# Optimization experiments

Hardware: AMD Instinct MI355X
Metric: run time of the kernel (lower is better)

## Reference

```python
import jax, jax.numpy as jnp
import numpy as np
from functools import partial

# Gate order along axis 0 of Wi/bi/Wh/bh: 0=r (input gate), 1=f (forget), 2=g (cell), 3=o (output)

def setup_inputs() -> dict:
    key = jax.random.key(0)
    ks = jax.random.split(key, 6)
    B, T, V, E, H, O = 64, 512, 32000, 256, 512, 1
    s_e, s_h = 1.0 / np.sqrt(E), 1.0 / np.sqrt(H)
    return {
        "input_words": jax.random.randint(ks[0], (B, T), 0, V, dtype=jnp.int64),
        "emb": jax.random.normal(ks[1], (V, E), dtype=jnp.float32) * 0.02,
        "Wi": jax.random.normal(ks[2], (4, H, E), dtype=jnp.float32) * s_e,
        "bi": jnp.zeros((4, H), dtype=jnp.float32),
        "Wh": jax.random.normal(ks[3], (4, H, H), dtype=jnp.float32) * s_h,
        "bh": jnp.zeros((4, H), dtype=jnp.float32),
        "Wfc": jax.random.normal(ks[4], (O, H), dtype=jnp.float32) * s_h,
        "bfc": jnp.zeros((O,), dtype=jnp.float32),
    }


def reference(input_words, emb, Wi, bi, Wh, bh, Wfc, bfc):
    B, T = input_words.shape
    H = Wh.shape[-1]
    x = emb[input_words]                     # [B, T, E]
    # Precompute input projections for all 4 gates, all timesteps: one big GEMM.
    xg = jnp.einsum('bte,ghe->tbgh', x, Wi) + bi  # [T, B, 4, H]

    def step(carry, xg_t):
        h, c = carry
        gates = xg_t + jnp.einsum('bk,ghk->bgh', h, Wh) + bh  # [B, 4, H]
        r = jax.nn.sigmoid(gates[:, 0])
        f = jax.nn.sigmoid(gates[:, 1])
        g = jnp.tanh(gates[:, 2])
        o = jax.nn.sigmoid(gates[:, 3])
        c = f * c + r * g
        h = o * jnp.tanh(c)
        return (h, c), None

    h0 = jnp.zeros((B, H), dtype=x.dtype)
    c0 = jnp.zeros((B, H), dtype=x.dtype)
    (h, c), _ = jax.lax.scan(step, (h0, c0), xg)
    out = jax.nn.sigmoid(h @ Wfc.T + bfc)    # [B, n_output]
    return (out, h)
```

## Files before the change

kernel.cpp:

```cpp
#include <hip/hip_runtime.h>
#include <hip/hip_bf16.h>

#define TB 512
#define NB 64
#define EE 256
#define HH 512
#define NG 4
#define GB 16
#define NBLK 16
#define NT 256
#define NCOLP 132

typedef __bf16 bf16_t;
typedef bf16_t bf16x8 __attribute__((ext_vector_type(8)));
typedef float  f32x4  __attribute__((ext_vector_type(4)));
typedef unsigned long long u64;

__device__ __forceinline__ float sigf(float x) { return 1.0f / (1.0f + __expf(-x)); }
__device__ __forceinline__ float tanhfast(float x) {
    float xc = fminf(fmaxf(x, -15.0f), 15.0f);
    float e  = __expf(2.0f * xc);
    return (e - 1.0f) / (e + 1.0f);
}
__device__ __forceinline__ unsigned bfbits(float f) {
    bf16_t h = (bf16_t)f;
    return (unsigned)__builtin_bit_cast(unsigned short, h);
}
__device__ __forceinline__ bf16x8 cvt8(float4 a, float4 b) {
    bf16x8 v;
    v[0]=(bf16_t)a.x; v[1]=(bf16_t)a.y; v[2]=(bf16_t)a.z; v[3]=(bf16_t)a.w;
    v[4]=(bf16_t)b.x; v[5]=(bf16_t)b.y; v[6]=(bf16_t)b.z; v[7]=(bf16_t)b.w;
    return v;
}

__global__ __launch_bounds__(NT, 1)
void lstm_persistent(const int* __restrict__ words,
                     const float* __restrict__ emb,
                     const float* __restrict__ Wi,
                     const float* __restrict__ bi,
                     const float* __restrict__ Wh,
                     const float* __restrict__ bh,
                     const float* __restrict__ Wfc,
                     const float* __restrict__ bfc,
                     float* __restrict__ out,
                     unsigned* __restrict__ flags,
                     bf16_t* __restrict__ hbuf)
{
    const int tid  = threadIdx.x;
    const int lane = tid & 63;
    const int wv   = tid >> 6;
    const int bg   = blockIdx.x & 3;
    const int ug   = blockIdx.x >> 2;
    const int kgrp = lane >> 4;
    const int cl   = lane & 15;

    __shared__ __align__(16) bf16_t h_lds[16][HH];
    __shared__ __align__(16) bf16_t x_lds[2][16][EE];
    __shared__ __align__(16) float  P_lds[16][NCOLP];

    for (int i = tid; i < 16*HH/2; i += NT) ((unsigned*)h_lds)[i] = 0u;

    bf16x8 whf[16][2];
    bf16x8 wif[8][2];
    float  biasn[2];
    #pragma unroll
    for (int nt = 0; nt < 2; ++nt) {
        int col = wv*32 + nt*16 + cl;
        int ul  = col >> 2, g = col & 3;
        int row = g*HH + ug*32 + ul;
        const float* wr = Wh + (size_t)row*HH;
        #pragma unroll
        for (int kt = 0; kt < 16; ++kt) {
            const float4* p = (const float4*)(wr + kt*32 + kgrp*8);
            whf[kt][nt] = cvt8(p[0], p[1]);
        }
        const float* wir = Wi + (size_t)row*EE;
        #pragma unroll
        for (int kt = 0; kt < 8; ++kt) {
            const float4* p = (const float4*)(wir + kt*32 + kgrp*8);
            wif[kt][nt] = cvt8(p[0], p[1]);
        }
        biasn[nt] = bi[row] + bh[row];
    }

    const int sb = tid & 15, sc = tid >> 4;
    const int swz = (sb & 7) << 3;

    {
        int word = words[(bg*GB + sb)*TB + 0];
        const float4* p = (const float4*)(emb + (size_t)word*EE + sc*16);
        float4 a=p[0], b=p[1], c=p[2], d=p[3];
        *(bf16x8*)&x_lds[0][sb][(sc*16    ) ^ swz] = cvt8(a, b);
        *(bf16x8*)&x_lds[0][sb][(sc*16 + 8) ^ swz] = cvt8(c, d);
    }

    unsigned* gflag = flags + bg*64;
    float c0 = 0.f, c1 = 0.f;
    __syncthreads();

    for (int t = 0; t < TB; ++t) {
        f32x4 acc0 = { biasn[0], biasn[0], biasn[0], biasn[0] };
        f32x4 acc1 = { biasn[1], biasn[1], biasn[1], biasn[1] };
        const bf16_t (*xl)[EE] = x_lds[t & 1];
        #pragma unroll
        for (int kt = 0; kt < 8; ++kt) {
            bf16x8 a = *(const bf16x8*)&xl[cl][(kt*32 + kgrp*8) ^ ((cl & 7) << 3)];
            acc0 = __builtin_amdgcn_mfma_f32_16x16x32_bf16(a, wif[kt][0], acc0, 0, 0, 0);
            acc1 = __builtin_amdgcn_mfma_f32_16x16x32_bf16(a, wif[kt][1], acc1, 0, 0, 0);
        }

        float4 xa, xb, xc, xd;
        const bool havex = (t + 1 < TB);
        if (havex) {
            int word = words[(bg*GB + sb)*TB + (t + 1)];
            const float4* p = (const float4*)(emb + (size_t)word*EE + sc*16);
            xa = p[0]; xb = p[1]; xc = p[2]; xd = p[3];
        }

        if (t > 0) {
            if (wv == 0) {
                unsigned tgt = (unsigned)t;
                for (;;) {
                    unsigned v = (lane < NBLK)
                        ? __hip_atomic_load(&gflag[lane], __ATOMIC_RELAXED, __HIP_MEMORY_SCOPE_AGENT)
                        : tgt;
                    if (__all((int)(v >= tgt))) break;
                    __builtin_amdgcn_s_sleep(1);
                }
                __builtin_amdgcn_fence(__ATOMIC_ACQUIRE, "agent");
            }
            __syncthreads();
        }

        if (t > 0) {
            const u64* src = (const u64*)(hbuf + (((size_t)((t & 1) ^ 1))*NB + bg*GB + sb)*HH + sc*32);
            u64 hr[8];
            #pragma unroll
            for (int q = 0; q < 8; ++q)
                hr[q] = __hip_atomic_load(src + q, __ATOMIC_RELAXED, __HIP_MEMORY_SCOPE_AGENT);
            #pragma unroll
            for (int q = 0; q < 4; ++q) {
                int phys = (sc*32 + q*8) ^ swz;
                *(u64*)&h_lds[sb][phys]     = hr[2*q];
                *(u64*)&h_lds[sb][phys + 4] = hr[2*q + 1];
            }
            __syncthreads();
        }

        #pragma unroll
        for (int kt = 0; kt < 16; ++kt) {
            bf16x8 a = *(const bf16x8*)&h_lds[cl][(kt*32 + kgrp*8) ^ ((cl & 7) << 3)];
            acc0 = __builtin_amdgcn_mfma_f32_16x16x32_bf16(a, whf[kt][0], acc0, 0, 0, 0);
            acc1 = __builtin_amdgcn_mfma_f32_16x16x32_bf16(a, whf[kt][1], acc1, 0, 0, 0);
        }

        if (havex) {
            bf16_t (*xn)[EE] = x_lds[(t + 1) & 1];
            *(bf16x8*)&xn[sb][(sc*16    ) ^ swz] = cvt8(xa, xb);
            *(bf16x8*)&xn[sb][(sc*16 + 8) ^ swz] = cvt8(xc, xd);
        }

        #pragma unroll
        for (int r = 0; r < 4; ++r) {
            P_lds[kgrp*4 + r][wv*32 + cl]      = acc0[r];
            P_lds[kgrp*4 + r][wv*32 + 16 + cl] = acc1[r];
        }
        __syncthreads();

        {
            int b = tid >> 5, u = tid & 31;
            float4 g0 = *(const float4*)&P_lds[b][u*4];
            float4 g1 = *(const float4*)&P_lds[b + 8][u*4];
            float r0 = sigf(g0.x), f0 = sigf(g0.y), z0 = tanhfast(g0.z), o0 = sigf(g0.w);
            float r1 = sigf(g1.x), f1 = sigf(g1.y), z1 = tanhfast(g1.z), o1 = sigf(g1.w);
            c0 = f0*c0 + r0*z0;
            c1 = f1*c1 + r1*z1;
            float h0 = o0*tanhfast(c0);
            float h1 = o1*tanhfast(c1);
            if (t == TB - 1) {
                out[64 + (size_t)(bg*GB + b    )*HH + ug*32 + u] = h0;
                out[64 + (size_t)(bg*GB + b + 8)*HH + ug*32 + u] = h1;
            }
            unsigned s0 = bfbits(h0), s1 = bfbits(h1);
            unsigned n0 = (unsigned)__shfl_down((int)s0, 1);
            unsigned n1 = (unsigned)__shfl_down((int)s1, 1);
            if (!(u & 1)) {
                size_t e0 = ((size_t)(t & 1)*NB + bg*GB + b    )*HH + ug*32 + u;
                size_t e1 = ((size_t)(t & 1)*NB + bg*GB + b + 8)*HH + ug*32 + u;
                __hip_atomic_store((unsigned*)(hbuf + e0), (s0 & 0xFFFFu) | (n0 << 16),
                                   __ATOMIC_RELAXED, __HIP_MEMORY_SCOPE_AGENT);
                __hip_atomic_store((unsigned*)(hbuf + e1), (s1 & 0xFFFFu) | (n1 << 16),
                                   __ATOMIC_RELAXED, __HIP_MEMORY_SCOPE_AGENT);
            }
        }

        __syncthreads();
        if (tid == 0) {
            __builtin_amdgcn_fence(__ATOMIC_RELEASE, "agent");
            __hip_atomic_store(&gflag[ug], (unsigned)(t + 1),
                               __ATOMIC_RELAXED, __HIP_MEMORY_SCOPE_AGENT);
        }
    }

    if (ug == 0) {
        if (wv == 0) {
            for (;;) {
                unsigned v = (lane < NBLK)
                    ? __hip_atomic_load(&gflag[lane], __ATOMIC_RELAXED, __HIP_MEMORY_SCOPE_AGENT)
                    : (unsigned)TB;
                if (__all((int)(v >= (unsigned)TB))) break;
                __builtin_amdgcn_s_sleep(1);
            }
            __builtin_amdgcn_fence(__ATOMIC_ACQUIRE, "agent");
        }
        __syncthreads();
        {
            int b = tid >> 4, seg = tid & 15;
            const u64* hp = (const u64*)(hbuf + ((size_t)1*NB + bg*GB + b)*HH + seg*32);
            float s = 0.f;
            #pragma unroll
            for (int q = 0; q < 8; ++q) {
                u64 w = __hip_atomic_load(hp + q, __ATOMIC_RELAXED, __HIP_MEMORY_SCOPE_AGENT);
                #pragma unroll
                for (int j = 0; j < 4; ++j) {
                    float hv = __uint_as_float((unsigned)((w >> (16*j)) & 0xFFFFu) << 16);
                    s += hv * Wfc[seg*32 + q*4 + j];
                }
            }
            #pragma unroll
            for (int d = 8; d >= 1; d >>= 1) s += __shfl_down(s, d, 16);
            if (seg == 0) out[bg*GB + b] = sigf(s + bfc[0]);
        }
    }
}

extern "C" void kernel_launch(void* const* d_in, const int* in_sizes, int n_in,
                              void* d_out, int out_size, void* d_ws, size_t ws_size,
                              hipStream_t stream) {
    (void)in_sizes; (void)n_in; (void)out_size; (void)ws_size;
    const int*   words = (const int*)d_in[0];
    const float* emb   = (const float*)d_in[1];
    const float* Wi    = (const float*)d_in[2];
    const float* bi    = (const float*)d_in[3];
    const float* Wh    = (const float*)d_in[4];
    const float* bh    = (const float*)d_in[5];
    const float* Wfc   = (const float*)d_in[6];
    const float* bfc   = (const float*)d_in[7];
    float* out = (float*)d_out;

    unsigned* flags = (unsigned*)d_ws;
    bf16_t*   hbuf  = (bf16_t*)((char*)d_ws + 4096);

    hipMemsetAsync(d_ws, 0, 4096 + (size_t)2*NB*HH*sizeof(bf16_t), stream);

    lstm_persistent<<<dim3(NG*NBLK), dim3(NT), 0, stream>>>(
        words, emb, Wi, bi, Wh, bh, Wfc, bfc, out, flags, hbuf);
}
```

Before: 2.423 ms.

## Replace per-block flag barrier with step-tagged hidden-state words

The separate flag array and its release/acquire handshake are removed. Each packed bf16 pair of h is now stored together with its timestep tag in one 64-bit atomic word, and consumers spin directly on the data they need until every tag matches. This drops one flag round-trip, a fence and a block barrier per timestep. In exchange it doubles the bytes of h exchanged through global memory, has every thread poll 16 words, and relies on tags alone for ordering instead of explicit fences.

```diff
diff --git a/kernel.cpp b/kernel.cpp
--- a/kernel.cpp
+++ b/kernel.cpp
@@ -7,14 +7,15 @@
 #define HH 512
 #define NG 4
 #define GB 16
-#define NBLK 16
 #define NT 256
 #define NCOLP 132
+#define NPAIR (HH/2)
 
 typedef __bf16 bf16_t;
 typedef bf16_t bf16x8 __attribute__((ext_vector_type(8)));
 typedef float  f32x4  __attribute__((ext_vector_type(4)));
 typedef unsigned long long u64;
+typedef unsigned u32;
 
 __device__ __forceinline__ float sigf(float x) { return 1.0f / (1.0f + __expf(-x)); }
 __device__ __forceinline__ float tanhfast(float x) {
@@ -43,8 +44,7 @@
                      const float* __restrict__ Wfc,
                      const float* __restrict__ bfc,
                      float* __restrict__ out,
-                     unsigned* __restrict__ flags,
-                     bf16_t* __restrict__ hbuf)
+                     u64* __restrict__ tagH)
 {
     const int tid  = threadIdx.x;
     const int lane = tid & 63;
@@ -94,7 +94,6 @@
         *(bf16x8*)&x_lds[0][sb][(sc*16 + 8) ^ swz] = cvt8(c, d);
     }
 
-    unsigned* gflag = flags + bg*64;
     float c0 = 0.f, c1 = 0.f;
     __syncthreads();
 
@@ -118,46 +117,41 @@
         }
 
         if (t > 0) {
-            if (wv == 0) {
-                unsigned tgt = (unsigned)t;
-                for (;;) {
-                    unsigned v = (lane < NBLK)
-                        ? __hip_atomic_load(&gflag[lane], __ATOMIC_RELAXED, __HIP_MEMORY_SCOPE_AGENT)
-                        : tgt;
-                    if (__all((int)(v >= tgt))) break;
-                    __builtin_amdgcn_s_sleep(1);
-                }
-                __builtin_amdgcn_fence(__ATOMIC_ACQUIRE, "agent");
-            }
-            __syncthreads();
-        }
-
-        if (t > 0) {
-            const u64* src = (const u64*)(hbuf + (((size_t)((t & 1) ^ 1))*NB + bg*GB + sb)*HH + sc*32);
-            u64 hr[8];
-            #pragma unroll
-            for (int q = 0; q < 8; ++q)
-                hr[q] = __hip_atomic_load(src + q, __ATOMIC_RELAXED, __HIP_MEMORY_SCOPE_AGENT);
-            #pragma unroll
-            for (int q = 0; q < 4; ++q) {
-                int phys = (sc*32 + q*8) ^ swz;
-                *(u64*)&h_lds[sb][phys]     = hr[2*q];
-                *(u64*)&h_lds[sb][phys + 4] = hr[2*q + 1];
-            }
-            __syncthreads();
-        }
+            const u64* src = tagH + ((size_t)((t & 1) ^ 1))*NB*NPAIR
+                                  + (size_t)(bg*GB + sb)*NPAIR + sc*16;
+            const u32 tag = (u32)t;
+            u64 hv[16];
+            for (;;) {
+                #pragma unroll
+                for (int j = 0; j < 16; ++j)
+                    hv[j] = __hip_atomic_load(src + j, __ATOMIC_RELAXED, __HIP_MEMORY_SCOPE_AGENT);
+                bool ok = true;
+                #pragma unroll
+                for (int j = 0; j < 16; ++j) ok &= ((u32)(hv[j] >> 32) == tag);
+                if (ok) break;
+                __builtin_amdgcn_s_sleep(1);
+            }
+            #pragma unroll
+            for (int j = 0; j < 16; j += 2) {
+                u64 pk = (u64)(u32)hv[j] | ((u64)(u32)hv[j+1] << 32);
+                int elem = sc*32 + 2*j;
+                int phys = ((elem & ~7) ^ swz) | (elem & 7);
+                *(u64*)&h_lds[sb][phys] = pk;
+            }
+        }
+
+        if (havex) {
+            bf16_t (*xn)[EE] = x_lds[(t + 1) & 1];
+            *(bf16x8*)&xn[sb][(sc*16    ) ^ swz] = cvt8(xa, xb);
+            *(bf16x8*)&xn[sb][(sc*16 + 8) ^ swz] = cvt8(xc, xd);
+        }
+        __syncthreads();
 
         #pragma unroll
         for (int kt = 0; kt < 16; ++kt) {
             bf16x8 a = *(const bf16x8*)&h_lds[cl][(kt*32 + kgrp*8) ^ ((cl & 7) << 3)];
             acc0 = __builtin_amdgcn_mfma_f32_16x16x32_bf16(a, whf[kt][0], acc0, 0, 0, 0);
             acc1 = __builtin_amdgcn_mfma_f32_16x16x32_bf16(a, whf[kt][1], acc1, 0, 0, 0);
-        }
-
-        if (havex) {
-            bf16_t (*xn)[EE] = x_lds[(t + 1) & 1];
-            *(bf16x8*)&xn[sb][(sc*16    ) ^ swz] = cvt8(xa, xb);
-            *(bf16x8*)&xn[sb][(sc*16 + 8) ^ swz] = cvt8(xc, xd);
         }
 
         #pragma unroll
@@ -185,51 +179,48 @@
             unsigned n0 = (unsigned)__shfl_down((int)s0, 1);
             unsigned n1 = (unsigned)__shfl_down((int)s1, 1);
             if (!(u & 1)) {
-                size_t e0 = ((size_t)(t & 1)*NB + bg*GB + b    )*HH + ug*32 + u;
-                size_t e1 = ((size_t)(t & 1)*NB + bg*GB + b + 8)*HH + ug*32 + u;
-                __hip_atomic_store((unsigned*)(hbuf + e0), (s0 & 0xFFFFu) | (n0 << 16),
-                                   __ATOMIC_RELAXED, __HIP_MEMORY_SCOPE_AGENT);
-                __hip_atomic_store((unsigned*)(hbuf + e1), (s1 & 0xFFFFu) | (n1 << 16),
-                                   __ATOMIC_RELAXED, __HIP_MEMORY_SCOPE_AGENT);
-            }
-        }
-
-        __syncthreads();
-        if (tid == 0) {
-            __builtin_amdgcn_fence(__ATOMIC_RELEASE, "agent");
-            __hip_atomic_store(&gflag[ug], (unsigned)(t + 1),
-                               __ATOMIC_RELAXED, __HIP_MEMORY_SCOPE_AGENT);
+                u64 tg = ((u64)(u32)(t + 1)) << 32;
+                u64 v0 = tg | (u64)((s0 & 0xFFFFu) | (n0 << 16));
+                u64 v1 = tg | (u64)((s1 & 0xFFFFu) | (n1 << 16));
+                size_t base = ((size_t)(t & 1))*NB*NPAIR;
+                size_t p0 = base + (size_t)(bg*GB + b    )*NPAIR + ug*16 + (u >> 1);
+                size_t p1 = base + (size_t)(bg*GB + b + 8)*NPAIR + ug*16 + (u >> 1);
+                __hip_atomic_store(tagH + p0, v0, __ATOMIC_RELAXED, __HIP_MEMORY_SCOPE_AGENT);
+                __hip_atomic_store(tagH + p1, v1, __ATOMIC_RELAXED, __HIP_MEMORY_SCOPE_AGENT);
+            }
         }
     }
 
     if (ug == 0) {
-        if (wv == 0) {
-            for (;;) {
-                unsigned v = (lane < NBLK)
-                    ? __hip_atomic_load(&gflag[lane], __ATOMIC_RELAXED, __HIP_MEMORY_SCOPE_AGENT)
-                    : (unsigned)TB;
-                if (__all((int)(v >= (unsigned)TB))) break;
-                __builtin_amdgcn_s_sleep(1);
-            }
-            __builtin_amdgcn_fence(__ATOMIC_ACQUIRE, "agent");
-        }
-        __syncthreads();
-        {
-            int b = tid >> 4, seg = tid & 15;
-            const u64* hp = (const u64*)(hbuf + ((size_t)1*NB + bg*GB + b)*HH + seg*32);
-            float s = 0.f;
-            #pragma unroll
-            for (int q = 0; q < 8; ++q) {
-                u64 w = __hip_atomic_load(hp + q, __ATOMIC_RELAXED, __HIP_MEMORY_SCOPE_AGENT);
-                #pragma unroll
-                for (int j = 0; j < 4; ++j) {
-                    float hv = __uint_as_float((unsigned)((w >> (16*j)) & 0xFFFFu) << 16);
-                    s += hv * Wfc[seg*32 + q*4 + j];
-                }
-            }
-            #pragma unroll
-            for (int d = 8; d >= 1; d >>= 1) s += __shfl_down(s, d, 16);
-            if (seg == 0) out[bg*GB + b] = sigf(s + bfc[0]);
+        const u64* src = tagH + ((size_t)((TB - 1) & 1))*NB*NPAIR
+                              + (size_t)(bg*GB + sb)*NPAIR + sc*16;
+        u64 hv[16];
+        for (;;) {
+            #pragma unroll
+            for (int j = 0; j < 16; ++j)
+                hv[j] = __hip_atomic_load(src + j, __ATOMIC_RELAXED, __HIP_MEMORY_SCOPE_AGENT);
+            bool ok = true;
+            #pragma unroll
+            for (int j = 0; j < 16; ++j) ok &= ((u32)(hv[j] >> 32) == (u32)TB);
+            if (ok) break;
+            __builtin_amdgcn_s_sleep(1);
+        }
+        float s = 0.f;
+        #pragma unroll
+        for (int j = 0; j < 16; ++j) {
+            u32 pl = (u32)hv[j];
+            float h0 = __uint_as_float((pl & 0xFFFFu) << 16);
+            float h1 = __uint_as_float(pl & 0xFFFF0000u);
+            s += h0 * Wfc[sc*32 + 2*j] + h1 * Wfc[sc*32 + 2*j + 1];
+        }
+        __syncthreads();
+        P_lds[sb][sc] = s;
+        __syncthreads();
+        if (tid < 16) {
+            float acc = 0.f;
+            #pragma unroll
+            for (int q = 0; q < 16; ++q) acc += P_lds[tid][q];
+            out[bg*GB + tid] = sigf(acc + bfc[0]);
         }
     }
 }
@@ -248,11 +239,10 @@
     const float* bfc   = (const float*)d_in[7];
     float* out = (float*)d_out;
 
-    unsigned* flags = (unsigned*)d_ws;
-    bf16_t*   hbuf  = (bf16_t*)((char*)d_ws + 4096);
-
-    hipMemsetAsync(d_ws, 0, 4096 + (size_t)2*NB*HH*sizeof(bf16_t), stream);
-
-    lstm_persistent<<<dim3(NG*NBLK), dim3(NT), 0, stream>>>(
-        words, emb, Wi, bi, Wh, bh, Wfc, bfc, out, flags, hbuf);
-}
+    u64* tagH = (u64*)d_ws;
+
+    hipMemsetAsync(d_ws, 0, (size_t)2*NB*NPAIR*sizeof(u64), stream);
+
+    lstm_persistent<<<dim3(NG*GB), dim3(NT), 0, stream>>>(
+        words, emb, Wi, bi, Wh, bh, Wfc, bfc, out, tagH);
+}
```

New measurement: 2.230 ms. -7.9%, faster.
